# Kernel optimization log

Measured on AMD Instinct MI355X. Metric: run time of the kernel, lower is better.

The kernel has to match this reference:

```python
import jax, jax.numpy as jnp
import numpy as np

N = 20000      # nodes
E = 320000     # edges (before self loops)
DIN = 64       # input feature dim
C = 256        # hidden_dim (per-head channels)
HEADS = 4
NEG_SLOPE_ATT = 0.2   # GATv2 leaky_relu slope
NEG_SLOPE = 0.01      # torch F.leaky_relu default


def setup_inputs() -> dict:
    key = jax.random.key(0)
    ks = jax.random.split(key, 32)
    def g(i, shape, fan_in):
        return jax.random.normal(ks[i], shape, jnp.float32) * (1.0 / np.sqrt(fan_in))
    inp = {}
    inp["x"] = jax.random.normal(ks[0], (N, DIN), jnp.float32)
    inp["src"] = jax.random.randint(ks[1], (E,), 0, N, jnp.int32)
    inp["dst"] = jax.random.randint(ks[2], (E,), 0, N, jnp.int32)
    # input layer
    inp["W_in"] = g(3, (DIN, C), DIN); inp["b_in"] = jnp.zeros((C,), jnp.float32)
    # conv1: in=256 -> heads=4, out=256, concat
    inp["Wl1"] = g(4, (C, HEADS * C), C); inp["bl1"] = jnp.zeros((HEADS * C,), jnp.float32)
    inp["Wr1"] = g(5, (C, HEADS * C), C); inp["br1"] = jnp.zeros((HEADS * C,), jnp.float32)
    inp["att1"] = g(6, (HEADS, C), C); inp["bias1"] = jnp.zeros((HEADS * C,), jnp.float32)
    # conv2: in=1024 -> heads=4, out=256, concat
    inp["Wl2"] = g(7, (HEADS * C, HEADS * C), HEADS * C); inp["bl2"] = jnp.zeros((HEADS * C,), jnp.float32)
    inp["Wr2"] = g(8, (HEADS * C, HEADS * C), HEADS * C); inp["br2"] = jnp.zeros((HEADS * C,), jnp.float32)
    inp["att2"] = g(9, (HEADS, C), C); inp["bias2"] = jnp.zeros((HEADS * C,), jnp.float32)
    # conv3: in=1024 -> heads=1, out=256, no concat
    inp["Wl3"] = g(10, (HEADS * C, C), HEADS * C); inp["bl3"] = jnp.zeros((C,), jnp.float32)
    inp["Wr3"] = g(11, (HEADS * C, C), HEADS * C); inp["br3"] = jnp.zeros((C,), jnp.float32)
    inp["att3"] = g(12, (1, C), C); inp["bias3"] = jnp.zeros((C,), jnp.float32)
    # output layer
    inp["W_out"] = g(13, (C, 1), C); inp["b_out"] = jnp.zeros((1,), jnp.float32)
    return inp


def _seg_softmax(scores, seg, n):
    # scores: [E, H] segment-wise softmax over dst node ids
    m = jax.ops.segment_max(scores, seg, num_segments=n)
    ex = jnp.exp(scores - m[seg])
    den = jax.ops.segment_sum(ex, seg, num_segments=n)
    return ex / den[seg]


def _gatv2(x, s, d, Wl, bl, Wr, br, att, bias, heads, concat):
    n = x.shape[0]
    c = att.shape[1]
    xl = (x @ Wl + bl).reshape(n, heads, c)  # messages (source side)
    xr = (x @ Wr + br).reshape(n, heads, c)  # target side
    e = jax.nn.leaky_relu(xl[s] + xr[d], NEG_SLOPE_ATT)          # [E, H, C]
    sc = jnp.einsum('ehc,hc->eh', e, att)                         # [E, H]
    alpha = _seg_softmax(sc, d, n)                                # [E, H]
    out = jax.ops.segment_sum(alpha[:, :, None] * xl[s], d, num_segments=n)  # [N, H, C]
    out = out.reshape(n, heads * c) if concat else out.mean(axis=1)
    return out + bias


def reference(x, src, dst, W_in, b_in, Wl1, bl1, Wr1, br1, att1, bias1,
              Wl2, bl2, Wr2, br2, att2, bias2, Wl3, bl3, Wr3, br3, att3, bias3,
              W_out, b_out):
    n = x.shape[0]
    loop = jnp.arange(n, dtype=src.dtype)
    s = jnp.concatenate([src, loop])  # add_self_loops=True (PyG default)
    d = jnp.concatenate([dst, loop])
    h = jax.nn.leaky_relu(x @ W_in + b_in, NEG_SLOPE)
    h1 = jax.nn.elu(_gatv2(h, s, d, Wl1, bl1, Wr1, br1, att1, bias1, HEADS, True))
    h2 = jax.nn.elu(_gatv2(h1, s, d, Wl2, bl2, Wr2, br2, att2, bias2, HEADS, True))
    h3 = _gatv2(h2, s, d, Wl3, bl3, Wr3, br3, att3, bias3, 1, False)
    out = jax.nn.leaky_relu(h3, NEG_SLOPE) + h
    logits = (out @ W_out + b_out).squeeze(-1)
    return logits
```

## Files before the change

kernel.cpp:

```cpp
#include <hip/hip_runtime.h>
#include <math.h>

#define NEG_ATT 0.2f
#define NEG 0.01f

typedef __attribute__((ext_vector_type(8))) short short8;
typedef __attribute__((ext_vector_type(4))) float f32x4;
typedef __attribute__((ext_vector_type(2))) float f32x2;

static __device__ __forceinline__ float lrelu(float x, float s) { return x > 0.f ? x : s * x; }
static __device__ __forceinline__ unsigned short f2b(float f) {
  union { float f; unsigned int i; } v; v.f = f;
  unsigned int r = (v.i + 0x7fffu + ((v.i >> 16) & 1u)) >> 16;
  return (unsigned short)r;
}
static __device__ __forceinline__ void up2x4(uint4 r, f32x2* v) {
  union { unsigned int i; float f; } t;
  t.i = r.x << 16;          v[0].x = t.f;
  t.i = r.x & 0xffff0000u;  v[0].y = t.f;
  t.i = r.y << 16;          v[1].x = t.f;
  t.i = r.y & 0xffff0000u;  v[1].y = t.f;
  t.i = r.z << 16;          v[2].x = t.f;
  t.i = r.z & 0xffff0000u;  v[2].y = t.f;
  t.i = r.w << 16;          v[3].x = t.f;
  t.i = r.w & 0xffff0000u;  v[3].y = t.f;
}

__global__ void hist_kernel(const int* __restrict__ dst, int* __restrict__ cnt, int E, int N) {
  int i = blockIdx.x * blockDim.x + threadIdx.x;
  int tot = E + N;
  if (i >= tot) return;
  int d = (i < E) ? dst[i] : (i - E);
  atomicAdd(&cnt[d], 1);
}

__global__ void scan1_kernel(const int* __restrict__ cnt, int* __restrict__ rowptr,
                             int* __restrict__ bsum, int n) {
  __shared__ int wsum[16];
  int t = threadIdx.x, lane = t & 63, wv = t >> 6;
  int i = blockIdx.x * 1024 + t;
  int orig = (i < n) ? cnt[i] : 0;
  int v = orig;
  #pragma unroll
  for (int off = 1; off < 64; off <<= 1) {
    int u = __shfl_up(v, off);
    if (lane >= off) v += u;
  }
  if (lane == 63) wsum[wv] = v;
  __syncthreads();
  if (t < 16) {
    int s = wsum[t];
    #pragma unroll
    for (int off = 1; off < 16; off <<= 1) {
      int u = __shfl_up(s, off);
      if (t >= off) s += u;
    }
    wsum[t] = s;
  }
  __syncthreads();
  int waveoff = (wv > 0) ? wsum[wv - 1] : 0;
  if (i < n) rowptr[i] = waveoff + v - orig;
  if (t == 1023) bsum[blockIdx.x] = wsum[15];
}

__global__ void scan2_kernel(int* __restrict__ rowptr, int* __restrict__ cursor,
                             const int* __restrict__ bsum, int n) {
  int t = threadIdx.x, b = blockIdx.x;
  int off = 0;
  for (int k = 0; k < b; ++k) off += bsum[k];
  int i = b * 1024 + t;
  if (i < n) { int e = rowptr[i] + off; rowptr[i] = e; cursor[i] = e; }
  if (b == (int)gridDim.x - 1 && t == 1023) rowptr[n] = off + bsum[b];
}

__global__ void fill_kernel(const int* __restrict__ src, const int* __restrict__ dst,
                            int* __restrict__ cursor, int* __restrict__ colsrc, int E, int N) {
  int i = blockIdx.x * blockDim.x + threadIdx.x;
  int tot = E + N;
  if (i >= tot) return;
  int d, s;
  if (i < E) { d = dst[i]; s = src[i]; } else { d = i - E; s = i - E; }
  int pos = atomicAdd(&cursor[d], 1);
  colsrc[pos] = s;
}

static __device__ __forceinline__ void do_transpose(
    const float* __restrict__ W, unsigned short* __restrict__ Wt,
    int K, int Ncol, int lbid, float (*t)[33]) {
  int nxb = Ncol >> 5;
  int bx = lbid % nxb, by = lbid / nxb;
  int n0 = bx * 32, k0 = by * 32;
  int tx = threadIdx.x & 31, ty = threadIdx.x >> 5;
  #pragma unroll
  for (int i = 0; i < 4; ++i)
    t[ty + i * 8][tx] = W[(size_t)(k0 + ty + i * 8) * Ncol + n0 + tx];
  __syncthreads();
  #pragma unroll
  for (int i = 0; i < 4; ++i)
    Wt[(size_t)(n0 + ty + i * 8) * K + k0 + tx] = f2b(t[tx][ty + i * 8]);
}

__global__ __launch_bounds__(256) void prep_all(
    const float* __restrict__ W_in,
    const float* __restrict__ Wl1, const float* __restrict__ Wr1,
    const float* __restrict__ Wl2, const float* __restrict__ Wr2,
    const float* __restrict__ Wl3, const float* __restrict__ Wr3,
    unsigned short* __restrict__ WtIn,
    unsigned short* __restrict__ WtL1, unsigned short* __restrict__ WtR1,
    unsigned short* __restrict__ WtL2, unsigned short* __restrict__ WtR2,
    unsigned short* __restrict__ WtL3, unsigned short* __restrict__ WtR3,
    const float* __restrict__ x, unsigned short* __restrict__ xbf, int nx_elems,
    const float* __restrict__ bl1, const float* __restrict__ br1,
    const float* __restrict__ bl2, const float* __restrict__ br2,
    const float* __restrict__ bl3, const float* __restrict__ br3,
    float* __restrict__ bLR1, float* __restrict__ bLR2, float* __restrict__ bLR3,
    int* __restrict__ cnt, int N) {
  __shared__ float t[32][33];
  int bid = blockIdx.x;
  if (bid < 16)        { do_transpose(W_in, WtIn, 64, 256, bid, t); return; }
  if (bid < 272)       { do_transpose(Wl1, WtL1, 256, 1024, bid - 16, t); return; }
  if (bid < 528)       { do_transpose(Wr1, WtR1, 256, 1024, bid - 272, t); return; }
  if (bid < 1552)      { do_transpose(Wl2, WtL2, 1024, 1024, bid - 528, t); return; }
  if (bid < 2576)      { do_transpose(Wr2, WtR2, 1024, 1024, bid - 1552, t); return; }
  if (bid < 2832)      { do_transpose(Wl3, WtL3, 1024, 256, bid - 2576, t); return; }
  if (bid < 3088)      { do_transpose(Wr3, WtR3, 1024, 256, bid - 2832, t); return; }
  if (bid < 3106) {
    int i = (bid - 3088) * 256 + threadIdx.x;
    if (i < 1024)      bLR1[i] = bl1[i];
    else if (i < 2048) bLR1[i] = br1[i - 1024];
    else if (i < 3072) bLR2[i - 2048] = bl2[i - 2048];
    else if (i < 4096) bLR2[i - 2048] = br2[i - 3072];
    else if (i < 4352) bLR3[i - 4096] = bl3[i - 4096];
    else if (i < 4608) bLR3[i - 4096] = br3[i - 4352];
    return;
  }
  int nbf2b = (nx_elems + 255) / 256;
  if (bid < 3106 + nbf2b) {
    int i = (bid - 3106) * 256 + threadIdx.x;
    if (i < nx_elems) xbf[i] = f2b(x[i]);
    return;
  }
  int i = (bid - 3106 - nbf2b) * 256 + threadIdx.x;
  if (i < N) cnt[i] = 0;
}

__global__ __launch_bounds__(256) void gemm_mfma(
    const unsigned short* __restrict__ A, const unsigned short* __restrict__ Bt,
    const float* __restrict__ bias, float* __restrict__ Cf, unsigned short* __restrict__ Cb,
    int M, int K, int ldcf, int ldcb, int act) {
  __shared__ __align__(16) unsigned short As[128 * 64];
  __shared__ __align__(16) unsigned short Bs[128 * 64];
  int tid = threadIdx.x;
  int wave = tid >> 6, lane = tid & 63;
  int wm = wave >> 1, wn = wave & 1;
  int quad = lane >> 4, l16 = lane & 15;
  int row0 = blockIdx.y * 128, col0 = blockIdx.x * 128;
  int r0 = tid >> 2, seg0 = tid & 3;
  int f0 = ((r0 & 1) << 2) | ((r0 >> 1) & 3);
  int wsl0 = r0 * 64 + ((seg0 ^ f0) * 8);
  int wsl1 = r0 * 64 + (((seg0 | 4) ^ f0) * 8);
  int wsl2 = wsl0 + 64 * 64;
  int wsl3 = wsl1 + 64 * 64;
  int flane = ((l16 & 1) << 2) | ((l16 >> 1) & 3);

  const unsigned short* gA = A + (size_t)(row0 + r0) * K + seg0 * 8;
  const unsigned short* gB = Bt + (size_t)(col0 + r0) * K + seg0 * 8;
  const size_t rstep = (size_t)64 * K;

  f32x4 acc[4][4];
  #pragma unroll
  for (int i = 0; i < 4; ++i)
    #pragma unroll
    for (int j = 0; j < 4; ++j)
      acc[i][j] = (f32x4){0.f, 0.f, 0.f, 0.f};

  uint4 pa0 = *(const uint4*)(gA);
  uint4 pa1 = *(const uint4*)(gA + 32);
  uint4 pa2 = *(const uint4*)(gA + rstep);
  uint4 pa3 = *(const uint4*)(gA + rstep + 32);
  uint4 pb0 = *(const uint4*)(gB);
  uint4 pb1 = *(const uint4*)(gB + 32);
  uint4 pb2 = *(const uint4*)(gB + rstep);
  uint4 pb3 = *(const uint4*)(gB + rstep + 32);

  for (int k0 = 0; k0 < K; k0 += 64) {
    *(uint4*)&As[wsl0] = pa0;
    *(uint4*)&As[wsl1] = pa1;
    *(uint4*)&As[wsl2] = pa2;
    *(uint4*)&As[wsl3] = pa3;
    *(uint4*)&Bs[wsl0] = pb0;
    *(uint4*)&Bs[wsl1] = pb1;
    *(uint4*)&Bs[wsl2] = pb2;
    *(uint4*)&Bs[wsl3] = pb3;
    __syncthreads();
    int kn = k0 + 64;
    if (kn < K) {
      pa0 = *(const uint4*)(gA + kn);
      pa1 = *(const uint4*)(gA + kn + 32);
      pa2 = *(const uint4*)(gA + kn + rstep);
      pa3 = *(const uint4*)(gA + kn + rstep + 32);
      pb0 = *(const uint4*)(gB + kn);
      pb1 = *(const uint4*)(gB + kn + 32);
      pb2 = *(const uint4*)(gB + kn + rstep);
      pb3 = *(const uint4*)(gB + kn + rstep + 32);
    }
    #pragma unroll
    for (int h = 0; h < 2; ++h) {
      short8 afr[4], bfr[4];
      #pragma unroll
      for (int t = 0; t < 4; ++t) {
        int pcs = (((h << 2) | quad) ^ flane) * 8;
        afr[t] = *(const short8*)&As[(wm * 64 + t * 16 + l16) * 64 + pcs];
        bfr[t] = *(const short8*)&Bs[(wn * 64 + t * 16 + l16) * 64 + pcs];
      }
      #pragma unroll
      for (int mt = 0; mt < 4; ++mt)
        #pragma unroll
        for (int nt = 0; nt < 4; ++nt)
          acc[mt][nt] = __builtin_amdgcn_mfma_f32_16x16x32_bf16(afr[mt], bfr[nt], acc[mt][nt], 0, 0, 0);
    }
    __syncthreads();
  }

  #pragma unroll
  for (int mt = 0; mt < 4; ++mt) {
    #pragma unroll
    for (int r = 0; r < 4; ++r) {
      int row = row0 + wm * 64 + mt * 16 + quad * 4 + r;
      if (row >= M) continue;
      #pragma unroll
      for (int nt = 0; nt < 4; ++nt) {
        int col = col0 + wn * 64 + nt * 16 + l16;
        float v = acc[mt][nt][r] + bias[col];
        if (act == 1) v = lrelu(v, NEG);
        if (Cf) Cf[(size_t)row * ldcf + col] = v;
        if (Cb) Cb[(size_t)row * ldcb + col] = f2b(v);
      }
    }
  }
}

__global__ __launch_bounds__(256) void gat_agg_h4(
    const unsigned short* __restrict__ xlr,
    const int* __restrict__ rowptr, const int* __restrict__ colsrc,
    const float* __restrict__ att, const float* __restrict__ bias,
    unsigned short* __restrict__ outb, int n) {
  int d = blockIdx.x;
  if (d >= n) return;
  int hd = threadIdx.x >> 6, ln = threadIdx.x & 63;
  int half = ln >> 5, l32 = ln & 31;
  int cbase = hd * 256 + l32 * 8;
  float a6[8], a4[8];
  f32x2 xr2[4];
  {
    float4 t0 = *(const float4*)(att + cbase);
    float4 t1 = *(const float4*)(att + cbase + 4);
    float a[8] = {t0.x, t0.y, t0.z, t0.w, t1.x, t1.y, t1.z, t1.w};
    #pragma unroll
    for (int c = 0; c < 8; ++c) { a6[c] = 0.6f * a[c]; a4[c] = 0.4f * a[c]; }
    uint4 r = *(const uint4*)(xlr + ((size_t)d << 11) + 1024 + cbase);
    up2x4(r, xr2);
  }
  float psp;
  {
    uint4 r = *(const uint4*)(xlr + ((size_t)d << 11) + cbase);
    f32x2 xs[4];
    up2x4(r, xs);
    f32x2 p2 = {0.f, 0.f};
    #pragma unroll
    for (int k = 0; k < 4; ++k) {
      f32x2 u = xs[k] + xr2[k];
      p2.x = fmaf(xs[k].x, a6[2 * k], p2.x);
      p2.x = fmaf(fabsf(u.x), a4[2 * k], p2.x);
      p2.y = fmaf(xs[k].y, a6[2 * k + 1], p2.y);
      p2.y = fmaf(fabsf(u.y), a4[2 * k + 1], p2.y);
    }
    psp = p2.x + p2.y;
    #pragma unroll
    for (int off = 16; off >= 1; off >>= 1) psp += __shfl_xor(psp, off);
  }
  float l = 0.f;
  f32x2 acc2[4];
  #pragma unroll
  for (int k = 0; k < 4; ++k) acc2[k] = (f32x2){0.f, 0.f};
  int beg = rowptr[d], end = rowptr[d + 1];
  for (int j = beg; j < end; j += 4) {
    int j0 = j + half, j1 = j + 2 + half;
    bool v0 = j0 < end, v1 = j1 < end;
    int s0 = colsrc[v0 ? j0 : beg];
    int s1 = colsrc[v1 ? j1 : beg];
    uint4 r0 = *(const uint4*)(xlr + ((size_t)s0 << 11) + cbase);
    uint4 r1 = *(const uint4*)(xlr + ((size_t)s1 << 11) + cbase);
    f32x2 x0[4], x1[4];
    up2x4(r0, x0);
    up2x4(r1, x1);
    float p0 = 0.f, p1 = 0.f;
    #pragma unroll
    for (int k = 0; k < 4; ++k) {
      f32x2 u0 = x0[k] + xr2[k];
      f32x2 u1 = x1[k] + xr2[k];
      p0 = fmaf(x0[k].x, a6[2 * k], p0);
      p0 = fmaf(fabsf(u0.x), a4[2 * k], p0);
      p0 = fmaf(x0[k].y, a6[2 * k + 1], p0);
      p0 = fmaf(fabsf(u0.y), a4[2 * k + 1], p0);
      p1 = fmaf(x1[k].x, a6[2 * k], p1);
      p1 = fmaf(fabsf(u1.x), a4[2 * k], p1);
      p1 = fmaf(x1[k].y, a6[2 * k + 1], p1);
      p1 = fmaf(fabsf(u1.y), a4[2 * k + 1], p1);
    }
    #pragma unroll
    for (int off = 16; off >= 1; off >>= 1) {
      p0 += __shfl_xor(p0, off);
      p1 += __shfl_xor(p1, off);
    }
    float w0 = v0 ? __expf(p0 - psp) : 0.f;
    float w1 = v1 ? __expf(p1 - psp) : 0.f;
    l += w0 + w1;
    f32x2 w02 = {w0, w0}, w12 = {w1, w1};
    #pragma unroll
    for (int k = 0; k < 4; ++k) {
      acc2[k] = w02 * x0[k] + acc2[k];
      acc2[k] = w12 * x1[k] + acc2[k];
    }
  }
  l += __shfl_xor(l, 32);
  float inv = 1.f / l;
  float4 b0 = *(const float4*)(bias + cbase);
  float4 b1 = *(const float4*)(bias + cbase + 4);
  float bb[8] = {b0.x, b0.y, b0.z, b0.w, b1.x, b1.y, b1.z, b1.w};
  unsigned int ou[4];
  #pragma unroll
  for (int k = 0; k < 4; ++k) {
    float sx = acc2[k].x + __shfl_xor(acc2[k].x, 32);
    float sy = acc2[k].y + __shfl_xor(acc2[k].y, 32);
    float vx = sx * inv + bb[2 * k];
    float vy = sy * inv + bb[2 * k + 1];
    vx = vx > 0.f ? vx : expm1f(vx);
    vy = vy > 0.f ? vy : expm1f(vy);
    ou[k] = (unsigned int)f2b(vx) | ((unsigned int)f2b(vy) << 16);
  }
  if (half == 0) {
    uint4 o = make_uint4(ou[0], ou[1], ou[2], ou[3]);
    *(uint4*)(outb + (size_t)d * 1024 + cbase) = o;
  }
}

__global__ __launch_bounds__(256) void gat_agg_h1_final(
    const unsigned short* __restrict__ xlr,
    const int* __restrict__ rowptr, const int* __restrict__ colsrc,
    const float* __restrict__ att, const float* __restrict__ bias,
    const float* __restrict__ h, const float* __restrict__ Wout,
    const float* __restrict__ bout, float* __restrict__ out, int n) {
  int wv = threadIdx.x >> 6, ln = threadIdx.x & 63;
  int d = blockIdx.x * 4 + wv;
  if (d >= n) return;
  int half = ln >> 5, l32 = ln & 31;
  int c0 = l32 * 8;
  float a6[8], a4[8];
  f32x2 xr2[4];
  {
    float4 t0 = *(const float4*)(att + c0);
    float4 t1 = *(const float4*)(att + c0 + 4);
    float a[8] = {t0.x, t0.y, t0.z, t0.w, t1.x, t1.y, t1.z, t1.w};
    #pragma unroll
    for (int c = 0; c < 8; ++c) { a6[c] = 0.6f * a[c]; a4[c] = 0.4f * a[c]; }
    uint4 r = *(const uint4*)(xlr + ((size_t)d << 9) + 256 + c0);
    up2x4(r, xr2);
  }
  float psp;
  {
    uint4 r = *(const uint4*)(xlr + ((size_t)d << 9) + c0);
    f32x2 xs[4];
    up2x4(r, xs);
    float p = 0.f;
    #pragma unroll
    for (int k = 0; k < 4; ++k) {
      f32x2 u = xs[k] + xr2[k];
      p = fmaf(xs[k].x, a6[2 * k], p);
      p = fmaf(fabsf(u.x), a4[2 * k], p);
      p = fmaf(xs[k].y, a6[2 * k + 1], p);
      p = fmaf(fabsf(u.y), a4[2 * k + 1], p);
    }
    psp = p;
    #pragma unroll
    for (int off = 16; off >= 1; off >>= 1) psp += __shfl_xor(psp, off);
  }
  float l = 0.f;
  f32x2 acc2[4];
  #pragma unroll
  for (int k = 0; k < 4; ++k) acc2[k] = (f32x2){0.f, 0.f};
  int beg = rowptr[d], end = rowptr[d + 1];
  for (int j = beg; j < end; j += 4) {
    int j0 = j + half, j1 = j + 2 + half;
    bool v0 = j0 < end, v1 = j1 < end;
    int s0 = colsrc[v0 ? j0 : beg];
    int s1 = colsrc[v1 ? j1 : beg];
    uint4 r0 = *(const uint4*)(xlr + ((size_t)s0 << 9) + c0);
    uint4 r1 = *(const uint4*)(xlr + ((size_t)s1 << 9) + c0);
    f32x2 x0[4], x1[4];
    up2x4(r0, x0);
    up2x4(r1, x1);
    float p0 = 0.f, p1 = 0.f;
    #pragma unroll
    for (int k = 0; k < 4; ++k) {
      f32x2 u0 = x0[k] + xr2[k];
      f32x2 u1 = x1[k] + xr2[k];
      p0 = fmaf(x0[k].x, a6[2 * k], p0);
      p0 = fmaf(fabsf(u0.x), a4[2 * k], p0);
      p0 = fmaf(x0[k].y, a6[2 * k + 1], p0);
      p0 = fmaf(fabsf(u0.y), a4[2 * k + 1], p0);
      p1 = fmaf(x1[k].x, a6[2 * k], p1);
      p1 = fmaf(fabsf(u1.x), a4[2 * k], p1);
      p1 = fmaf(x1[k].y, a6[2 * k + 1], p1);
      p1 = fmaf(fabsf(u1.y), a4[2 * k + 1], p1);
    }
    #pragma unroll
    for (int off = 16; off >= 1; off >>= 1) {
      p0 += __shfl_xor(p0, off);
      p1 += __shfl_xor(p1, off);
    }
    float w0 = v0 ? __expf(p0 - psp) : 0.f;
    float w1 = v1 ? __expf(p1 - psp) : 0.f;
    l += w0 + w1;
    f32x2 w02 = {w0, w0}, w12 = {w1, w1};
    #pragma unroll
    for (int k = 0; k < 4; ++k) {
      acc2[k] = w02 * x0[k] + acc2[k];
      acc2[k] = w12 * x1[k] + acc2[k];
    }
  }
  l += __shfl_xor(l, 32);
  float inv = 1.f / l;
  float4 b0 = *(const float4*)(bias + c0);
  float4 b1 = *(const float4*)(bias + c0 + 4);
  float bb[8] = {b0.x, b0.y, b0.z, b0.w, b1.x, b1.y, b1.z, b1.w};
  float4 h0 = *(const float4*)(h + (size_t)d * 256 + c0);
  float4 h1v = *(const float4*)(h + (size_t)d * 256 + c0 + 4);
  float hh[8] = {h0.x, h0.y, h0.z, h0.w, h1v.x, h1v.y, h1v.z, h1v.w};
  float4 w0v = *(const float4*)(Wout + c0);
  float4 w1v = *(const float4*)(Wout + c0 + 4);
  float ww[8] = {w0v.x, w0v.y, w0v.z, w0v.w, w1v.x, w1v.y, w1v.z, w1v.w};
  float v = 0.f;
  #pragma unroll
  for (int k = 0; k < 4; ++k) {
    float sx = acc2[k].x + __shfl_xor(acc2[k].x, 32);
    float sy = acc2[k].y + __shfl_xor(acc2[k].y, 32);
    float h3x = sx * inv + bb[2 * k];
    float h3y = sy * inv + bb[2 * k + 1];
    v = fmaf(lrelu(h3x, NEG) + hh[2 * k], ww[2 * k], v);
    v = fmaf(lrelu(h3y, NEG) + hh[2 * k + 1], ww[2 * k + 1], v);
  }
  #pragma unroll
  for (int off = 16; off >= 1; off >>= 1) v += __shfl_xor(v, off);
  if (ln == 0) out[d] = v + bout[0];
}

extern "C" void kernel_launch(void* const* d_in, const int* in_sizes, int n_in,
                              void* d_out, int out_size, void* d_ws, size_t ws_size,
                              hipStream_t stream) {
  const float* x    = (const float*)d_in[0];
  const int*   src  = (const int*)d_in[1];
  const int*   dst  = (const int*)d_in[2];
  const float* W_in = (const float*)d_in[3];
  const float* b_in = (const float*)d_in[4];
  const float* Wl1 = (const float*)d_in[5];  const float* bl1 = (const float*)d_in[6];
  const float* Wr1 = (const float*)d_in[7];  const float* br1 = (const float*)d_in[8];
  const float* att1 = (const float*)d_in[9]; const float* bias1 = (const float*)d_in[10];
  const float* Wl2 = (const float*)d_in[11]; const float* bl2 = (const float*)d_in[12];
  const float* Wr2 = (const float*)d_in[13]; const float* br2 = (const float*)d_in[14];
  const float* att2 = (const float*)d_in[15]; const float* bias2 = (const float*)d_in[16];
  const float* Wl3 = (const float*)d_in[17]; const float* bl3 = (const float*)d_in[18];
  const float* Wr3 = (const float*)d_in[19]; const float* br3 = (const float*)d_in[20];
  const float* att3 = (const float*)d_in[21]; const float* bias3 = (const float*)d_in[22];
  const float* W_out = (const float*)d_in[23]; const float* b_out = (const float*)d_in[24];

  const int N = in_sizes[0] / 64;
  const int E = in_sizes[1];
  const int NP = ((N + 127) / 128) * 128;
  float* out = (float*)d_out;

  char* p = (char*)d_ws;
  float* h    = (float*)p;            p += (size_t)N * 256 * 4;
  unsigned short* hbf   = (unsigned short*)p; p += (size_t)NP * 256 * 2;
  unsigned short* h12bf = (unsigned short*)p; p += (size_t)NP * 1024 * 2;
  unsigned short* xlr   = (unsigned short*)p; p += (size_t)N * 2048 * 2;
  unsigned short* WtIn  = (unsigned short*)p; p += (size_t)256 * 64 * 2;
  unsigned short* WtLR1 = (unsigned short*)p; p += (size_t)2048 * 256 * 2;
  unsigned short* WtLR2 = (unsigned short*)p; p += (size_t)2048 * 1024 * 2;
  unsigned short* WtLR3 = (unsigned short*)p; p += (size_t)512 * 1024 * 2;
  float* bLR1 = (float*)p;            p += (size_t)2048 * 4;
  float* bLR2 = (float*)p;            p += (size_t)2048 * 4;
  float* bLR3 = (float*)p;            p += (size_t)512 * 4;
  int* bsum   = (int*)p;              p += (size_t)64 * 4;
  int* cnt    = (int*)p;              p += (size_t)N * 4;
  int* cursor = (int*)p;              p += (size_t)N * 4;
  int* rowptr = (int*)p;              p += (size_t)(N + 1) * 4;
  int* colsrc = (int*)p;
  unsigned short* xbf = xlr;

  const int tot = E + N;
  dim3 blk(256);

  int nbf2b = (N * 64 + 255) / 256;
  int nz = (N + 255) / 256;
  prep_all<<<3106 + nbf2b + nz, blk, 0, stream>>>(
      W_in, Wl1, Wr1, Wl2, Wr2, Wl3, Wr3,
      WtIn, WtLR1, WtLR1 + (size_t)1024 * 256,
      WtLR2, WtLR2 + (size_t)1024 * 1024,
      WtLR3, WtLR3 + (size_t)256 * 1024,
      x, xbf, N * 64,
      bl1, br1, bl2, br2, bl3, br3, bLR1, bLR2, bLR3,
      cnt, N);

  int nsb = (N + 1023) / 1024;
  hist_kernel<<<(tot + 255) / 256, blk, 0, stream>>>(dst, cnt, E, N);
  scan1_kernel<<<nsb, 1024, 0, stream>>>(cnt, rowptr, bsum, N);
  scan2_kernel<<<nsb, 1024, 0, stream>>>(rowptr, cursor, bsum, N);
  fill_kernel<<<(tot + 255) / 256, blk, 0, stream>>>(src, dst, cursor, colsrc, E, N);

  int gy = NP / 128;
  int gagg4 = N;
  int gagg1 = (N + 3) / 4;

  gemm_mfma<<<dim3(2, gy), blk, 0, stream>>>(xbf, WtIn, b_in, h, hbf, N, 64, 256, 256, 1);

  gemm_mfma<<<dim3(16, gy), blk, 0, stream>>>(hbf, WtLR1, bLR1, nullptr, xlr, N, 256, 0, 2048, 0);
  gat_agg_h4<<<gagg4, blk, 0, stream>>>(xlr, rowptr, colsrc, att1, bias1, h12bf, N);

  gemm_mfma<<<dim3(16, gy), blk, 0, stream>>>(h12bf, WtLR2, bLR2, nullptr, xlr, N, 1024, 0, 2048, 0);
  gat_agg_h4<<<gagg4, blk, 0, stream>>>(xlr, rowptr, colsrc, att2, bias2, h12bf, N);

  gemm_mfma<<<dim3(4, gy), blk, 0, stream>>>(h12bf, WtLR3, bLR3, nullptr, xlr, N, 1024, 0, 512, 0);
  gat_agg_h1_final<<<gagg1, blk, 0, stream>>>(xlr, rowptr, colsrc, att3, bias3,
                                              h, W_out, b_out, out, N);
}
```

Measured before the change: 652.0 us.

## Precompute per-node linear attention term in GEMM epilogue for GATv2 aggregation

```diff
diff --git a/kernel.cpp b/kernel.cpp
--- a/kernel.cpp
+++ b/kernel.cpp
@@ -114,7 +114,7 @@
     const float* __restrict__ bl2, const float* __restrict__ br2,
     const float* __restrict__ bl3, const float* __restrict__ br3,
     float* __restrict__ bLR1, float* __restrict__ bLR2, float* __restrict__ bLR3,
-    int* __restrict__ cnt, int N) {
+    int* __restrict__ cnt, float* __restrict__ dotsAll, int N) {
   __shared__ float t[32][33];
   int bid = blockIdx.x;
   if (bid < 16)        { do_transpose(W_in, WtIn, 64, 256, bid, t); return; }
@@ -142,11 +142,13 @@
   }
   int i = (bid - 3106 - nbf2b) * 256 + threadIdx.x;
   if (i < N) cnt[i] = 0;
+  else if (i < N + 8 * N) dotsAll[i - N] = 0.f;
 }
 
 __global__ __launch_bounds__(256) void gemm_mfma(
     const unsigned short* __restrict__ A, const unsigned short* __restrict__ Bt,
     const float* __restrict__ bias, float* __restrict__ Cf, unsigned short* __restrict__ Cb,
+    const float* __restrict__ att, float* __restrict__ dots,
     int M, int K, int ldcf, int ldcb, int act) {
   __shared__ __align__(16) unsigned short As[128 * 64];
   __shared__ __align__(16) unsigned short Bs[128 * 64];
@@ -222,12 +224,21 @@
     __syncthreads();
   }
 
+  bool dodot = (dots != nullptr) && (col0 < 1024);
+  int hd = col0 >> 8;
+  float a6e[4] = {0.f, 0.f, 0.f, 0.f};
+  if (dodot) {
+    #pragma unroll
+    for (int nt = 0; nt < 4; ++nt)
+      a6e[nt] = 0.6f * att[hd * 256 + (col0 & 255) + wn * 64 + nt * 16 + l16];
+  }
   #pragma unroll
   for (int mt = 0; mt < 4; ++mt) {
     #pragma unroll
     for (int r = 0; r < 4; ++r) {
       int row = row0 + wm * 64 + mt * 16 + quad * 4 + r;
       if (row >= M) continue;
+      float dp = 0.f;
       #pragma unroll
       for (int nt = 0; nt < 4; ++nt) {
         int col = col0 + wn * 64 + nt * 16 + l16;
@@ -235,13 +246,21 @@
         if (act == 1) v = lrelu(v, NEG);
         if (Cf) Cf[(size_t)row * ldcf + col] = v;
         if (Cb) Cb[(size_t)row * ldcb + col] = f2b(v);
+        dp = fmaf(v, a6e[nt], dp);
       }
+      if (dodot) {
+        dp += __shfl_xor(dp, 1);
+        dp += __shfl_xor(dp, 2);
+        dp += __shfl_xor(dp, 4);
+        dp += __shfl_xor(dp, 8);
+        if (l16 == 0) atomicAdd(&dots[row * 4 + hd], dp);
+      }
     }
   }
 }
 
 __global__ __launch_bounds__(256) void gat_agg_h4(
-    const unsigned short* __restrict__ xlr,
+    const unsigned short* __restrict__ xlr, const float* __restrict__ dots,
     const int* __restrict__ rowptr, const int* __restrict__ colsrc,
     const float* __restrict__ att, const float* __restrict__ bias,
     unsigned short* __restrict__ outb, int n) {
@@ -250,34 +269,32 @@
   int hd = threadIdx.x >> 6, ln = threadIdx.x & 63;
   int half = ln >> 5, l32 = ln & 31;
   int cbase = hd * 256 + l32 * 8;
-  float a6[8], a4[8];
+  float a4[8];
   f32x2 xr2[4];
   {
     float4 t0 = *(const float4*)(att + cbase);
     float4 t1 = *(const float4*)(att + cbase + 4);
     float a[8] = {t0.x, t0.y, t0.z, t0.w, t1.x, t1.y, t1.z, t1.w};
     #pragma unroll
-    for (int c = 0; c < 8; ++c) { a6[c] = 0.6f * a[c]; a4[c] = 0.4f * a[c]; }
+    for (int c = 0; c < 8; ++c) a4[c] = 0.4f * a[c];
     uint4 r = *(const uint4*)(xlr + ((size_t)d << 11) + 1024 + cbase);
     up2x4(r, xr2);
   }
-  float psp;
+  float psb;
   {
     uint4 r = *(const uint4*)(xlr + ((size_t)d << 11) + cbase);
     f32x2 xs[4];
     up2x4(r, xs);
-    f32x2 p2 = {0.f, 0.f};
+    float p = 0.f;
     #pragma unroll
     for (int k = 0; k < 4; ++k) {
       f32x2 u = xs[k] + xr2[k];
-      p2.x = fmaf(xs[k].x, a6[2 * k], p2.x);
-      p2.x = fmaf(fabsf(u.x), a4[2 * k], p2.x);
-      p2.y = fmaf(xs[k].y, a6[2 * k + 1], p2.y);
-      p2.y = fmaf(fabsf(u.y), a4[2 * k + 1], p2.y);
-    }
-    psp = p2.x + p2.y;
-    #pragma unroll
-    for (int off = 16; off >= 1; off >>= 1) psp += __shfl_xor(psp, off);
+      p = fmaf(fabsf(u.x), a4[2 * k], p);
+      p = fmaf(fabsf(u.y), a4[2 * k + 1], p);
+    }
+    #pragma unroll
+    for (int off = 16; off >= 1; off >>= 1) p += __shfl_xor(p, off);
+    psb = p + dots[d * 4 + hd];
   }
   float l = 0.f;
   f32x2 acc2[4];
@@ -289,6 +306,8 @@
     bool v0 = j0 < end, v1 = j1 < end;
     int s0 = colsrc[v0 ? j0 : beg];
     int s1 = colsrc[v1 ? j1 : beg];
+    float ds0 = dots[s0 * 4 + hd];
+    float ds1 = dots[s1 * 4 + hd];
     uint4 r0 = *(const uint4*)(xlr + ((size_t)s0 << 11) + cbase);
     uint4 r1 = *(const uint4*)(xlr + ((size_t)s1 << 11) + cbase);
     f32x2 x0[4], x1[4];
@@ -299,13 +318,9 @@
     for (int k = 0; k < 4; ++k) {
       f32x2 u0 = x0[k] + xr2[k];
       f32x2 u1 = x1[k] + xr2[k];
-      p0 = fmaf(x0[k].x, a6[2 * k], p0);
       p0 = fmaf(fabsf(u0.x), a4[2 * k], p0);
-      p0 = fmaf(x0[k].y, a6[2 * k + 1], p0);
       p0 = fmaf(fabsf(u0.y), a4[2 * k + 1], p0);
-      p1 = fmaf(x1[k].x, a6[2 * k], p1);
       p1 = fmaf(fabsf(u1.x), a4[2 * k], p1);
-      p1 = fmaf(x1[k].y, a6[2 * k + 1], p1);
       p1 = fmaf(fabsf(u1.y), a4[2 * k + 1], p1);
     }
     #pragma unroll
@@ -313,8 +328,8 @@
       p0 += __shfl_xor(p0, off);
       p1 += __shfl_xor(p1, off);
     }
-    float w0 = v0 ? __expf(p0 - psp) : 0.f;
-    float w1 = v1 ? __expf(p1 - psp) : 0.f;
+    float w0 = v0 ? __expf(p0 + ds0 - psb) : 0.f;
+    float w1 = v1 ? __expf(p1 + ds1 - psb) : 0.f;
     l += w0 + w1;
     f32x2 w02 = {w0, w0}, w12 = {w1, w1};
     #pragma unroll
@@ -491,6 +506,8 @@
   float* bLR1 = (float*)p;            p += (size_t)2048 * 4;
   float* bLR2 = (float*)p;            p += (size_t)2048 * 4;
   float* bLR3 = (float*)p;            p += (size_t)512 * 4;
+  float* dots1 = (float*)p;           p += (size_t)N * 4 * 4;
+  float* dots2 = (float*)p;           p += (size_t)N * 4 * 4;
   int* bsum   = (int*)p;              p += (size_t)64 * 4;
   int* cnt    = (int*)p;              p += (size_t)N * 4;
   int* cursor = (int*)p;              p += (size_t)N * 4;
@@ -502,7 +519,7 @@
   dim3 blk(256);
 
   int nbf2b = (N * 64 + 255) / 256;
-  int nz = (N + 255) / 256;
+  int nz = (9 * N + 255) / 256;
   prep_all<<<3106 + nbf2b + nz, blk, 0, stream>>>(
       W_in, Wl1, Wr1, Wl2, Wr2, Wl3, Wr3,
       WtIn, WtLR1, WtLR1 + (size_t)1024 * 256,
@@ -510,7 +527,7 @@
       WtLR3, WtLR3 + (size_t)256 * 1024,
       x, xbf, N * 64,
       bl1, br1, bl2, br2, bl3, br3, bLR1, bLR2, bLR3,
-      cnt, N);
+      cnt, dots1, N);
 
   int nsb = (N + 1023) / 1024;
   hist_kernel<<<(tot + 255) / 256, blk, 0, stream>>>(dst, cnt, E, N);
@@ -522,15 +539,19 @@
   int gagg4 = N;
   int gagg1 = (N + 3) / 4;
 
-  gemm_mfma<<<dim3(2, gy), blk, 0, stream>>>(xbf, WtIn, b_in, h, hbf, N, 64, 256, 256, 1);
-
-  gemm_mfma<<<dim3(16, gy), blk, 0, stream>>>(hbf, WtLR1, bLR1, nullptr, xlr, N, 256, 0, 2048, 0);
-  gat_agg_h4<<<gagg4, blk, 0, stream>>>(xlr, rowptr, colsrc, att1, bias1, h12bf, N);
-
-  gemm_mfma<<<dim3(16, gy), blk, 0, stream>>>(h12bf, WtLR2, bLR2, nullptr, xlr, N, 1024, 0, 2048, 0);
-  gat_agg_h4<<<gagg4, blk, 0, stream>>>(xlr, rowptr, colsrc, att2, bias2, h12bf, N);
-
-  gemm_mfma<<<dim3(4, gy), blk, 0, stream>>>(h12bf, WtLR3, bLR3, nullptr, xlr, N, 1024, 0, 512, 0);
+  gemm_mfma<<<dim3(2, gy), blk, 0, stream>>>(xbf, WtIn, b_in, h, hbf,
+                                             nullptr, nullptr, N, 64, 256, 256, 1);
+
+  gemm_mfma<<<dim3(16, gy), blk, 0, stream>>>(hbf, WtLR1, bLR1, nullptr, xlr,
+                                              att1, dots1, N, 256, 0, 2048, 0);
+  gat_agg_h4<<<gagg4, blk, 0, stream>>>(xlr, dots1, rowptr, colsrc, att1, bias1, h12bf, N);
+
+  gemm_mfma<<<dim3(16, gy), blk, 0, stream>>>(h12bf, WtLR2, bLR2, nullptr, xlr,
+                                              att2, dots2, N, 1024, 0, 2048, 0);
+  gat_agg_h4<<<gagg4, blk, 0, stream>>>(xlr, dots2, rowptr, colsrc, att2, bias2, h12bf, N);
+
+  gemm_mfma<<<dim3(4, gy), blk, 0, stream>>>(h12bf, WtLR3, bLR3, nullptr, xlr,
+                                             nullptr, nullptr, N, 1024, 0, 512, 0);
   gat_agg_h1_final<<<gagg1, blk, 0, stream>>>(xlr, rowptr, colsrc, att3, bias3,
                                               h, W_out, b_out, out, N);
 }
```

Result: slower. 708.8 us (+8.7%).
